# Optimization experiments

Hardware: AMD Instinct MI355X
Metric: run time of the kernel (lower is better)

## Reference

```python
import jax, jax.numpy as jnp
import numpy as np
import math

B, N, XD, ED, H = 8, 128, 256, 128, 8
DF = XD // H
FFX, FFE = 1024, 512


def _lin(x, w, b):
    return x @ w + b


def _ln(x, g, b):
    m = x.mean(-1, keepdims=True)
    v = ((x - m) ** 2).mean(-1, keepdims=True)
    return (x - m) / jnp.sqrt(v + 1e-5) * g + b


def setup_inputs() -> dict:
    key = jax.random.key(0)
    ks = jax.random.split(key, 16)
    d = {}
    d['x'] = jax.random.normal(ks[0], (B, N, XD), jnp.float32)
    d['e'] = jax.random.normal(ks[1], (B, N, N, ED), jnp.float32)
    wspecs = [('wq', (XD, XD)), ('wk', (XD, XD)), ('wv', (XD, XD)),
              ('wem', (ED, XD)), ('wea', (ED, XD)), ('wxo', (XD, XD)),
              ('weo', (XD, ED)), ('wx1', (XD, FFX)), ('wx2', (FFX, XD)),
              ('we1', (ED, FFE)), ('we2', (FFE, ED))]
    for i, (name, shp) in enumerate(wspecs):
        d[name] = jax.random.normal(ks[2 + i % 14], shp, jnp.float32) * 0.02
        d[name] = jax.random.normal(jax.random.fold_in(key, i + 10), shp, jnp.float32) * 0.02
    for name, dim in [('bq', XD), ('bk', XD), ('bv', XD), ('bem', XD), ('bea', XD),
                      ('bxo', XD), ('beo', ED), ('bx1', FFX), ('bx2', XD),
                      ('be1', FFE), ('be2', ED)]:
        d[name] = jnp.zeros((dim,), jnp.float32)
    d['gnx'] = jnp.ones((XD,), jnp.float32)
    d['bnx'] = jnp.zeros((XD,), jnp.float32)
    d['gne'] = jnp.ones((ED,), jnp.float32)
    d['bne'] = jnp.zeros((ED,), jnp.float32)
    return d


def reference(x, e, wq, wk, wv, wem, wea, wxo, weo, wx1, wx2, we1, we2,
              bq, bk, bv, bem, bea, bxo, beo, bx1, bx2, be1, be2,
              gnx, bnx, gne, bne):
    # --- NodeEdgeBlock ---
    Q = _lin(x, wq, bq).reshape(B, N, H, DF)
    K = _lin(x, wk, bk).reshape(B, N, H, DF)
    # per-channel outer product: (B, N_i, N_j, H, DF)
    Y = Q[:, :, None] * K[:, None] / math.sqrt(DF)
    E1 = _lin(e, wem, bem).reshape(B, N, N, H, DF)
    E2 = _lin(e, wea, bea).reshape(B, N, N, H, DF)
    Y = Y * (E1 + 1.0) + E2
    newE = _lin(Y.reshape(B, N, N, XD), weo, beo)
    attn = jax.nn.softmax(Y, axis=1)  # softmax over source-node axis i
    V = _lin(x, wv, bv := bv if False else bv).reshape(B, N, H, DF) if False else _lin(x, wv, bv).reshape(B, N, H, DF)
    wV = (attn * V[:, None]).sum(axis=1).reshape(B, N, XD)
    newX = _lin(wV, wxo, bxo)

    # --- FF blocks (dropout=0 => identity); note the SAME norm (norm2) is applied twice,
    # and the second residual uses the pre-norm input, matching the torch code. ---
    def ff(inp, new, w1, b1, w2, b2, g, bn):
        h = _ln(inp + new, g, bn)
        h = jax.nn.relu(_lin(h, w1, b1))
        h = _lin(h, w2, b2)
        return _ln(inp + h, g, bn)

    x_out = ff(x, newX, wx1, bx1, wx2, bx2, gnx, bnx)
    e_out = ff(e, newE, we1, be1, we2, be2, gne, bne)
    return (x_out, e_out)
```

## Files before the change

### kernel.cpp

```cpp
#include <hip/hip_runtime.h>


#define RSQRT_DF 0.17677669529663687f

typedef __attribute__((ext_vector_type(8))) short short8;
typedef __attribute__((ext_vector_type(4))) short short4v;
typedef __attribute__((ext_vector_type(4))) float f32x4;

__device__ __forceinline__ short f2bs(float f) {
    unsigned u = __float_as_uint(f);
    unsigned r = u + 0x7FFFu + ((u >> 16) & 1u);
    return (short)(r >> 16);
}
__device__ __forceinline__ float bs2f(short s) {
    return __uint_as_float(((unsigned)(unsigned short)s) << 16);
}

struct PackArgs {
    const float* W[11];
    short* Wp[11];
    int kdiv[11];
    int N[11];
    int start[12];
};

__global__ __launch_bounds__(256) void pack_all(PackArgs pa) {
    int g = blockIdx.x * 256 + threadIdx.x;
    if (g >= pa.start[11]) return;
    int i = 0;
    while (g >= pa.start[i + 1]) ++i;
    int local = g - pa.start[i];
    int kdiv = pa.kdiv[i], N = pa.N[i];
    int lane = local & 63, rest = local >> 6;
    int kb = rest % kdiv, nt = rest / kdiv;
    int n = nt * 16 + (lane & 15);
    int k0 = kb * 32 + ((lane >> 4) << 3);
    const float* W = pa.W[i];
    short8 v;
#pragma unroll
    for (int j = 0; j < 8; ++j) v[j] = f2bs(W[(size_t)(k0 + j) * N + n]);
    *(short8*)(pa.Wp[i] + (size_t)local * 8) = v;
}

__global__ __launch_bounds__(256) void qk_gemm(
    const float* __restrict__ x,
    const short* __restrict__ wqP, const short* __restrict__ wkP,
    const float* __restrict__ bq, const float* __restrict__ bk,
    float* __restrict__ Qb, float* __restrict__ Kb) {
    __shared__ short sXb[16 * 264];
    const int t = threadIdx.x, wave = t >> 6, lane = t & 63;
    const int quad = lane >> 4, l15 = lane & 15;
    const int m0 = (blockIdx.x & 63) * 16;
    const int isK = blockIdx.x >> 6;
    const short* wP = isK ? wkP : wqP;
    const float* bp = isK ? bk : bq;
    float* outp = isK ? Kb : Qb;

    const float4* x4 = (const float4*)(x + (size_t)m0 * 256);
    for (int g = t; g < 1024; g += 256) {
        float4 v = x4[g];
        int row = g >> 6, col4 = (g & 63) * 4;
        short4v sv = {f2bs(v.x), f2bs(v.y), f2bs(v.z), f2bs(v.w)};
        *(short4v*)(sXb + row * 264 + col4) = sv;
    }
    __syncthreads();

#pragma unroll 2
    for (int p = 0; p < 4; ++p) {
        int nt = wave * 4 + p;
        f32x4 acc = (f32x4){0.f, 0.f, 0.f, 0.f};
        const short* aB = sXb + l15 * 264 + quad * 8;
        const short* bB = wP + ((size_t)(nt * 8) * 64 + lane) * 8;
#pragma unroll
        for (int kb = 0; kb < 8; ++kb) {
            short8 a = *(const short8*)(aB + kb * 32);
            short8 w = *(const short8*)(bB + (size_t)kb * 512);
            acc = __builtin_amdgcn_mfma_f32_16x16x32_bf16(a, w, acc, 0, 0, 0);
        }
        int col = nt * 16 + l15;
        float bvv = bp[col];
#pragma unroll
        for (int r = 0; r < 4; ++r)
            outp[(size_t)(m0 + quad * 4 + r) * 256 + col] = acc[r] + bvv;
    }
}

__global__ __launch_bounds__(512, 3) void fused_main(
    const float* __restrict__ x, const float* __restrict__ e,
    const float* __restrict__ Qb, const float* __restrict__ Kb,
    const short* __restrict__ wvP, const short* __restrict__ wxoP,
    const short* __restrict__ wx1P, const short* __restrict__ wx2P,
    const short* __restrict__ wemP, const short* __restrict__ weaP,
    const short* __restrict__ weoP, const short* __restrict__ we1P,
    const short* __restrict__ we2P,
    const float* __restrict__ bv, const float* __restrict__ bxo,
    const float* __restrict__ bx1, const float* __restrict__ bx2,
    const float* __restrict__ bem, const float* __restrict__ bea,
    const float* __restrict__ beo, const float* __restrict__ be1,
    const float* __restrict__ be2,
    const float* __restrict__ gnx, const float* __restrict__ bnx,
    const float* __restrict__ gne, const float* __restrict__ bne,
    float* __restrict__ xout, float* __restrict__ eout) {
    __shared__ __align__(16) char ldsbuf[68608];
    const int t = threadIdx.x, wave = t >> 6, lane = t & 63;
    const int quad = lane >> 4, l15 = lane & 15;

    if (blockIdx.x < 32) {
        short* sXb  = (short*)ldsbuf;
        short* sVb  = (short*)(ldsbuf + 16896);
        short* sTbx = (short*)(ldsbuf + 33792);
        short* sRx  = (short*)(ldsbuf + 50688);
        short* sH1x = (short*)(ldsbuf + 50688);
        short* sH2x = (short*)(ldsbuf + 50688);
        const int m0 = blockIdx.x * 32;

        const float4* x4 = (const float4*)(x + (size_t)m0 * 256);
        for (int g = t; g < 2048; g += 512) {
            float4 v = x4[g];
            int row = g >> 6, col4 = (g & 63) * 4;
            short4v sv = {f2bs(v.x), f2bs(v.y), f2bs(v.z), f2bs(v.w)};
            *(short4v*)(sXb + row * 264 + col4) = sv;
        }
        __syncthreads();

#pragma unroll
        for (int ntl = 0; ntl < 2; ++ntl) {
            const int nt = wave * 2 + ntl;
            const short* bB = wvP + ((size_t)(nt * 8) * 64 + lane) * 8;
            short8 w[8];
#pragma unroll
            for (int kb = 0; kb < 8; ++kb) w[kb] = *(const short8*)(bB + (size_t)kb * 512);
            const int col = nt * 16 + l15;
            const float bvv = bv[col];
#pragma unroll
            for (int mt = 0; mt < 2; ++mt) {
                f32x4 acc = (f32x4){0.f, 0.f, 0.f, 0.f};
#pragma unroll
                for (int kb = 0; kb < 8; ++kb) {
                    short8 a = *(const short8*)(sXb + (mt * 16 + l15) * 264 + quad * 8 + kb * 32);
                    acc = __builtin_amdgcn_mfma_f32_16x16x32_bf16(a, w[kb], acc, 0, 0, 0);
                }
#pragma unroll
                for (int r = 0; r < 4; ++r)
                    sVb[(mt * 16 + quad * 4 + r) * 264 + col] = f2bs(acc[r] + bvv);
            }
        }
        __syncthreads();

#pragma unroll
        for (int ntl = 0; ntl < 2; ++ntl) {
            const int nt = wave * 2 + ntl;
            const short* bB = wxoP + ((size_t)(nt * 8) * 64 + lane) * 8;
            short8 w[8];
#pragma unroll
            for (int kb = 0; kb < 8; ++kb) w[kb] = *(const short8*)(bB + (size_t)kb * 512);
            const int col = nt * 16 + l15;
            const float bvv = bxo[col];
#pragma unroll
            for (int mt = 0; mt < 2; ++mt) {
                f32x4 acc = (f32x4){0.f, 0.f, 0.f, 0.f};
#pragma unroll
                for (int kb = 0; kb < 8; ++kb) {
                    short8 a = *(const short8*)(sVb + (mt * 16 + l15) * 264 + quad * 8 + kb * 32);
                    acc = __builtin_amdgcn_mfma_f32_16x16x32_bf16(a, w[kb], acc, 0, 0, 0);
                }
#pragma unroll
                for (int r = 0; r < 4; ++r)
                    sRx[(mt * 16 + quad * 4 + r) * 264 + col] = f2bs(acc[r] + bvv);
            }
        }
        __syncthreads();

        for (int rr = 0; rr < 4; ++rr) {
            int row = wave * 4 + rr;
            float v[4];
            float s1 = 0.f, s2 = 0.f;
#pragma unroll
            for (int k = 0; k < 4; ++k) {
                v[k] = bs2f(sXb[row * 264 + lane + 64 * k]) + bs2f(sRx[row * 264 + lane + 64 * k]);
                s1 += v[k]; s2 += v[k] * v[k];
            }
            for (int off = 32; off; off >>= 1) {
                s1 += __shfl_down(s1, off);
                s2 += __shfl_down(s2, off);
            }
            s1 = __shfl(s1, 0); s2 = __shfl(s2, 0);
            float mean = s1 * (1.f / 256.f);
            float var = s2 * (1.f / 256.f) - mean * mean;
            float rstd = rsqrtf(var + 1e-5f);
#pragma unroll
            for (int k = 0; k < 4; ++k)
                sTbx[row * 264 + lane + 64 * k] =
                    f2bs((v[k] - mean) * rstd * gnx[lane + 64 * k] + bnx[lane + 64 * k]);
        }
        __syncthreads();

        f32x4 accEx[2][2];
#pragma unroll
        for (int i = 0; i < 2; ++i)
#pragma unroll
            for (int j = 0; j < 2; ++j) accEx[i][j] = (f32x4){0.f, 0.f, 0.f, 0.f};

        for (int q = 0; q < 4; ++q) {
#pragma unroll
            for (int ntl = 0; ntl < 2; ++ntl) {
                const int ntg = q * 16 + wave * 2 + ntl;
                const short* bB = wx1P + ((size_t)(ntg * 8) * 64 + lane) * 8;
                short8 w[8];
#pragma unroll
                for (int kb = 0; kb < 8; ++kb) w[kb] = *(const short8*)(bB + (size_t)kb * 512);
                const int coll = (wave * 2 + ntl) * 16 + l15;
                const float bvv = bx1[ntg * 16 + l15];
#pragma unroll
                for (int mt = 0; mt < 2; ++mt) {
                    f32x4 acc = (f32x4){0.f, 0.f, 0.f, 0.f};
#pragma unroll
                    for (int kb = 0; kb < 8; ++kb) {
                        short8 a = *(const short8*)(sTbx + (mt * 16 + l15) * 264 + quad * 8 + kb * 32);
                        acc = __builtin_amdgcn_mfma_f32_16x16x32_bf16(a, w[kb], acc, 0, 0, 0);
                    }
#pragma unroll
                    for (int r = 0; r < 4; ++r)
                        sH1x[(mt * 16 + quad * 4 + r) * 264 + coll] = f2bs(fmaxf(acc[r] + bvv, 0.f));
                }
            }
            __syncthreads();
#pragma unroll
            for (int ntl = 0; ntl < 2; ++ntl) {
                const int nt = wave * 2 + ntl;
                const short* bB = wx2P + ((size_t)(nt * 32 + q * 8) * 64 + lane) * 8;
                short8 w[8];
#pragma unroll
                for (int kb = 0; kb < 8; ++kb) w[kb] = *(const short8*)(bB + (size_t)kb * 512);
#pragma unroll
                for (int mt = 0; mt < 2; ++mt) {
#pragma unroll
                    for (int kb = 0; kb < 8; ++kb) {
                        short8 a = *(const short8*)(sH1x + (mt * 16 + l15) * 264 + quad * 8 + kb * 32);
                        accEx[ntl][mt] = __builtin_amdgcn_mfma_f32_16x16x32_bf16(a, w[kb], accEx[ntl][mt], 0, 0, 0);
                    }
                }
            }
            __syncthreads();
        }
#pragma unroll
        for (int ntl = 0; ntl < 2; ++ntl)
#pragma unroll
            for (int mt = 0; mt < 2; ++mt) {
                const int col = (wave * 2 + ntl) * 16 + l15;
                const float bvv = bx2[col];
#pragma unroll
                for (int r = 0; r < 4; ++r)
                    sH2x[(mt * 16 + quad * 4 + r) * 264 + col] = f2bs(accEx[ntl][mt][r] + bvv);
            }
        __syncthreads();

        for (int rr = 0; rr < 4; ++rr) {
            int row = wave * 4 + rr;
            float v[4];
            float s1 = 0.f, s2 = 0.f;
#pragma unroll
            for (int k = 0; k < 4; ++k) {
                v[k] = bs2f(sXb[row * 264 + lane + 64 * k]) + bs2f(sH2x[row * 264 + lane + 64 * k]);
                s1 += v[k]; s2 += v[k] * v[k];
            }
            for (int off = 32; off; off >>= 1) {
                s1 += __shfl_down(s1, off);
                s2 += __shfl_down(s2, off);
            }
            s1 = __shfl(s1, 0); s2 = __shfl(s2, 0);
            float mean = s1 * (1.f / 256.f);
            float var = s2 * (1.f / 256.f) - mean * mean;
            float rstd = rsqrtf(var + 1e-5f);
#pragma unroll
            for (int k = 0; k < 4; ++k)
                xout[(size_t)(m0 + row) * 256 + lane + 64 * k] =
                    (v[k] - mean) * rstd * gnx[lane + 64 * k] + bnx[lane + 64 * k];
        }
        return;
    }

    short* sEb = (short*)ldsbuf;
    short* sYb = (short*)(ldsbuf + 17408);
    short* sTb = (short*)(ldsbuf + 17408);
    float* sH2 = (float*)(ldsbuf + 17408);
    short* sR  = (short*)(ldsbuf + 51200);
    short* sH1 = (short*)(ldsbuf + 51200);

    const int r0 = (blockIdx.x - 32) * 64;
    const int b = r0 >> 14;
    const int j0 = r0 & 127;

    {
        const float4* e4 = (const float4*)(e + (size_t)r0 * 128);
        for (int g = t; g < 2048; g += 512) {
            float4 v = e4[g];
            int row = g >> 5, col4 = (g & 31) * 4;
            short4v sv = {f2bs(v.x), f2bs(v.y), f2bs(v.z), f2bs(v.w)};
            *(short4v*)(sEb + row * 136 + col4) = sv;
        }
    }
    __syncthreads();

#pragma unroll
    for (int ntl = 0; ntl < 2; ++ntl) {
        const int nt = wave * 2 + ntl;
        const short* b1 = wemP + ((size_t)(nt * 4) * 64 + lane) * 8;
        const short* b2 = weaP + ((size_t)(nt * 4) * 64 + lane) * 8;
        short8 w1[4], w2[4];
#pragma unroll
        for (int kb = 0; kb < 4; ++kb) {
            w1[kb] = *(const short8*)(b1 + (size_t)kb * 512);
            w2[kb] = *(const short8*)(b2 + (size_t)kb * 512);
        }
        const int col = nt * 16 + l15;
        const float bm = bem[col], ba = bea[col];
        const float q = Qb[(size_t)(r0 >> 7) * 256 + col] * RSQRT_DF;
#pragma unroll
        for (int mt = 0; mt < 4; ++mt) {
            const float* kp = Kb + (size_t)((b << 7) + j0 + mt * 16 + quad * 4) * 256 + col;
            float kv[4];
#pragma unroll
            for (int r = 0; r < 4; ++r) kv[r] = kp[(size_t)r * 256];
            f32x4 a1 = (f32x4){0.f, 0.f, 0.f, 0.f};
            f32x4 a2 = (f32x4){0.f, 0.f, 0.f, 0.f};
#pragma unroll
            for (int kb = 0; kb < 4; ++kb) {
                short8 a = *(const short8*)(sEb + (mt * 16 + l15) * 136 + quad * 8 + kb * 32);
                a1 = __builtin_amdgcn_mfma_f32_16x16x32_bf16(a, w1[kb], a1, 0, 0, 0);
                a2 = __builtin_amdgcn_mfma_f32_16x16x32_bf16(a, w2[kb], a2, 0, 0, 0);
            }
#pragma unroll
            for (int r = 0; r < 4; ++r) {
                int row = mt * 16 + quad * 4 + r;
                float y = q * kv[r] * (a1[r] + bm + 1.0f) + (a2[r] + ba);
                sYb[row * 264 + col] = f2bs(y);
            }
        }
    }
    __syncthreads();

    {
        const int nt = wave;
        const short* bB = weoP + ((size_t)(nt * 8) * 64 + lane) * 8;
        short8 w[8];
#pragma unroll
        for (int kb = 0; kb < 8; ++kb) w[kb] = *(const short8*)(bB + (size_t)kb * 512);
        const int col = nt * 16 + l15;
        const float bo = beo[col];
#pragma unroll
        for (int mt = 0; mt < 4; ++mt) {
            f32x4 acc = (f32x4){0.f, 0.f, 0.f, 0.f};
#pragma unroll
            for (int kb = 0; kb < 8; ++kb) {
                short8 a = *(const short8*)(sYb + (mt * 16 + l15) * 264 + quad * 8 + kb * 32);
                acc = __builtin_amdgcn_mfma_f32_16x16x32_bf16(a, w[kb], acc, 0, 0, 0);
            }
#pragma unroll
            for (int r = 0; r < 4; ++r)
                sR[(mt * 16 + quad * 4 + r) * 136 + col] = f2bs(acc[r] + bo);
        }
    }
    __syncthreads();

    {
        float g0 = gne[lane], g1 = gne[lane + 64];
        float bn0 = bne[lane], bn1 = bne[lane + 64];
        for (int rr = 0; rr < 8; ++rr) {
            int row = wave * 8 + rr;
            float v0 = bs2f(sEb[row * 136 + lane]) + bs2f(sR[row * 136 + lane]);
            float v1 = bs2f(sEb[row * 136 + lane + 64]) + bs2f(sR[row * 136 + lane + 64]);
            float s1 = v0 + v1, s2 = v0 * v0 + v1 * v1;
            for (int off = 32; off; off >>= 1) {
                s1 += __shfl_down(s1, off);
                s2 += __shfl_down(s2, off);
            }
            s1 = __shfl(s1, 0); s2 = __shfl(s2, 0);
            float mean = s1 * 0.0078125f;
            float var = s2 * 0.0078125f - mean * mean;
            float rstd = rsqrtf(var + 1e-5f);
            sTb[row * 136 + lane]      = f2bs((v0 - mean) * rstd * g0 + bn0);
            sTb[row * 136 + lane + 64] = f2bs((v1 - mean) * rstd * g1 + bn1);
        }
    }
    __syncthreads();

    f32x4 accE[4];
#pragma unroll
    for (int p = 0; p < 4; ++p) accE[p] = (f32x4){0.f, 0.f, 0.f, 0.f};

    for (int q = 0; q < 4; ++q) {
        {
            const int ntg = q * 8 + wave;
            const short* bB = we1P + ((size_t)(ntg * 4) * 64 + lane) * 8;
            short8 w[4];
#pragma unroll
            for (int kb = 0; kb < 4; ++kb) w[kb] = *(const short8*)(bB + (size_t)kb * 512);
            const int coll = wave * 16 + l15;
            const float bvv = be1[ntg * 16 + l15];
#pragma unroll
            for (int mt = 0; mt < 4; ++mt) {
                f32x4 acc = (f32x4){0.f, 0.f, 0.f, 0.f};
#pragma unroll
                for (int kb = 0; kb < 4; ++kb) {
                    short8 a = *(const short8*)(sTb + (mt * 16 + l15) * 136 + quad * 8 + kb * 32);
                    acc = __builtin_amdgcn_mfma_f32_16x16x32_bf16(a, w[kb], acc, 0, 0, 0);
                }
#pragma unroll
                for (int r = 0; r < 4; ++r)
                    sH1[(mt * 16 + quad * 4 + r) * 136 + coll] = f2bs(fmaxf(acc[r] + bvv, 0.f));
            }
        }
        __syncthreads();
        {
            const int nt = wave;
            const short* bB = we2P + ((size_t)(nt * 16 + q * 4) * 64 + lane) * 8;
            short8 w[4];
#pragma unroll
            for (int kb = 0; kb < 4; ++kb) w[kb] = *(const short8*)(bB + (size_t)kb * 512);
#pragma unroll
            for (int mt = 0; mt < 4; ++mt) {
#pragma unroll
                for (int kb = 0; kb < 4; ++kb) {
                    short8 a = *(const short8*)(sH1 + (mt * 16 + l15) * 136 + quad * 8 + kb * 32);
                    accE[mt] = __builtin_amdgcn_mfma_f32_16x16x32_bf16(a, w[kb], accE[mt], 0, 0, 0);
                }
            }
        }
        __syncthreads();
    }
    {
        const int col = wave * 16 + l15;
        const float bvv = be2[col];
#pragma unroll
        for (int mt = 0; mt < 4; ++mt)
#pragma unroll
            for (int r = 0; r < 4; ++r)
                sH2[(mt * 16 + quad * 4 + r) * 132 + col] = accE[mt][r] + bvv;
    }
    __syncthreads();

    {
        float g0 = gne[lane], g1 = gne[lane + 64];
        float bn0 = bne[lane], bn1 = bne[lane + 64];
        for (int rr = 0; rr < 8; ++rr) {
            int row = wave * 8 + rr;
            float v0 = bs2f(sEb[row * 136 + lane]) + sH2[row * 132 + lane];
            float v1 = bs2f(sEb[row * 136 + lane + 64]) + sH2[row * 132 + lane + 64];
            float s1 = v0 + v1, s2 = v0 * v0 + v1 * v1;
            for (int off = 32; off; off >>= 1) {
                s1 += __shfl_down(s1, off);
                s2 += __shfl_down(s2, off);
            }
            s1 = __shfl(s1, 0); s2 = __shfl(s2, 0);
            float mean = s1 * 0.0078125f;
            float var = s2 * 0.0078125f - mean * mean;
            float rstd = rsqrtf(var + 1e-5f);
            size_t o = (size_t)(r0 + row) * 128;
            eout[o + lane]      = (v0 - mean) * rstd * g0 + bn0;
            eout[o + lane + 64] = (v1 - mean) * rstd * g1 + bn1;
        }
    }
}

extern "C" void kernel_launch(void* const* d_in, const int* in_sizes, int n_in,
                              void* d_out, int out_size, void* d_ws, size_t ws_size,
                              hipStream_t stream) {
    const float* x   = (const float*)d_in[0];
    const float* e   = (const float*)d_in[1];
    const float* wq  = (const float*)d_in[2];
    const float* wk  = (const float*)d_in[3];
    const float* wv  = (const float*)d_in[4];
    const float* wem = (const float*)d_in[5];
    const float* wea = (const float*)d_in[6];
    const float* wxo = (const float*)d_in[7];
    const float* weo = (const float*)d_in[8];
    const float* wx1 = (const float*)d_in[9];
    const float* wx2 = (const float*)d_in[10];
    const float* we1 = (const float*)d_in[11];
    const float* we2 = (const float*)d_in[12];
    const float* bq  = (const float*)d_in[13];
    const float* bk  = (const float*)d_in[14];
    const float* bv  = (const float*)d_in[15];
    const float* bem = (const float*)d_in[16];
    const float* bea = (const float*)d_in[17];
    const float* bxo = (const float*)d_in[18];
    const float* beo = (const float*)d_in[19];
    const float* bx1 = (const float*)d_in[20];
    const float* bx2 = (const float*)d_in[21];
    const float* be1 = (const float*)d_in[22];
    const float* be2 = (const float*)d_in[23];
    const float* gnx = (const float*)d_in[24];
    const float* bnx = (const float*)d_in[25];
    const float* gne = (const float*)d_in[26];
    const float* bne = (const float*)d_in[27];

    float* out = (float*)d_out;

    float* ws = (float*)d_ws;
    float* Qb = ws;
    float* Kb = Qb + 262144;
    short* base = (short*)(Kb + 262144);
    short* wqP  = base;
    short* wkP  = wqP + 65536;
    short* wvP  = wkP + 65536;
    short* wxoP = wvP + 65536;
    short* wx1P = wxoP + 65536;
    short* wx2P = wx1P + 262144;
    short* wemP = wx2P + 262144;
    short* weaP = wemP + 32768;
    short* weoP = weaP + 32768;
    short* we1P = weoP + 32768;
    short* we2P = we1P + 65536;

    PackArgs pa;
    const float* Ws[11] = {wq, wk, wv, wxo, wx1, wx2, wem, wea, weo, we1, we2};
    short* Wps[11] = {wqP, wkP, wvP, wxoP, wx1P, wx2P, wemP, weaP, weoP, we1P, we2P};
    int Ks[11] = {256, 256, 256, 256, 256, 1024, 128, 128, 256, 128, 512};
    int Ns[11] = {256, 256, 256, 256, 1024, 256, 256, 256, 128, 512, 128};
    int acc = 0;
    for (int i = 0; i < 11; ++i) {
        pa.W[i] = Ws[i];
        pa.Wp[i] = Wps[i];
        pa.kdiv[i] = Ks[i] >> 5;
        pa.N[i] = Ns[i];
        pa.start[i] = acc;
        acc += (Ns[i] >> 4) * (Ks[i] >> 5) * 64;
    }
    pa.start[11] = acc;
    pack_all<<<(acc + 255) / 256, 256, 0, stream>>>(pa);

    qk_gemm<<<128, 256, 0, stream>>>(x, wqP, wkP, bq, bk, Qb, Kb);

    fused_main<<<2080, 512, 0, stream>>>(
        x, e, Qb, Kb, wvP, wxoP, wx1P, wx2P, wemP, weaP, weoP, we1P, we2P,
        bv, bxo, bx1, bx2, bem, bea, beo, be1, be2,
        gnx, bnx, gne, bne, out, out + 262144);
}
```

Baseline: 296.8 us.

## Hoist edge-path weight loads and software-prefetch FFN weights across stages

Loads the wem/wea/weo weight fragments and the per-column constants into registers before the e-tile load, so their global latency overlaps with the staging of e into LDS. The E1/E2 loop is reordered to run over row tiles with both column tiles at once, which shares each A-fragment LDS read across four MFMAs. The FFN loop now double-buffers we1/we2 fragments, fetching the next chunk's weights while the current MFMAs run. The cost is much higher register pressure (dozens of short8 values live at once), which could lower occupancy or cause spills.

After: 326.3 us. 10.0% more time.

```diff
diff --git a/kernel.cpp b/kernel.cpp
--- a/kernel.cpp
+++ b/kernel.cpp
@@ -291,6 +291,36 @@
     const int b = r0 >> 14;
     const int j0 = r0 & 127;
 
+    const int ntA = wave * 2, ntB = wave * 2 + 1;
+    const int colA = ntA * 16 + l15, colB = ntB * 16 + l15;
+    short8 w1A[4], w2A[4], w1B[4], w2B[4];
+    {
+        const short* p1A = wemP + ((size_t)(ntA * 4) * 64 + lane) * 8;
+        const short* p2A = weaP + ((size_t)(ntA * 4) * 64 + lane) * 8;
+        const short* p1B = wemP + ((size_t)(ntB * 4) * 64 + lane) * 8;
+        const short* p2B = weaP + ((size_t)(ntB * 4) * 64 + lane) * 8;
+#pragma unroll
+        for (int kb = 0; kb < 4; ++kb) {
+            w1A[kb] = *(const short8*)(p1A + (size_t)kb * 512);
+            w2A[kb] = *(const short8*)(p2A + (size_t)kb * 512);
+            w1B[kb] = *(const short8*)(p1B + (size_t)kb * 512);
+            w2B[kb] = *(const short8*)(p2B + (size_t)kb * 512);
+        }
+    }
+    short8 wC[8];
+    {
+        const short* pC = weoP + ((size_t)(wave * 8) * 64 + lane) * 8;
+#pragma unroll
+        for (int kb = 0; kb < 8; ++kb) wC[kb] = *(const short8*)(pC + (size_t)kb * 512);
+    }
+    const float qA = Qb[(size_t)(r0 >> 7) * 256 + colA] * RSQRT_DF;
+    const float qB = Qb[(size_t)(r0 >> 7) * 256 + colB] * RSQRT_DF;
+    const float bmA = bem[colA], baA = bea[colA];
+    const float bmB = bem[colB], baB = bea[colB];
+    const float boC = beo[wave * 16 + l15];
+    const float g0 = gne[lane], g1 = gne[lane + 64];
+    const float bn0 = bne[lane], bn1 = bne[lane + 64];
+
     {
         const float4* e4 = (const float4*)(e + (size_t)r0 * 128);
         for (int g = t; g < 2048; g += 512) {
@@ -303,85 +333,77 @@
     __syncthreads();
 
 #pragma unroll
-    for (int ntl = 0; ntl < 2; ++ntl) {
-        const int nt = wave * 2 + ntl;
-        const short* b1 = wemP + ((size_t)(nt * 4) * 64 + lane) * 8;
-        const short* b2 = weaP + ((size_t)(nt * 4) * 64 + lane) * 8;
-        short8 w1[4], w2[4];
+    for (int mt = 0; mt < 4; ++mt) {
+        const float* kpA = Kb + (size_t)((b << 7) + j0 + mt * 16 + quad * 4) * 256 + colA;
+        const float* kpB = Kb + (size_t)((b << 7) + j0 + mt * 16 + quad * 4) * 256 + colB;
+        float kvA[4], kvB[4];
+#pragma unroll
+        for (int r = 0; r < 4; ++r) {
+            kvA[r] = kpA[(size_t)r * 256];
+            kvB[r] = kpB[(size_t)r * 256];
+        }
+        short8 aE[4];
+#pragma unroll
+        for (int kb = 0; kb < 4; ++kb)
+            aE[kb] = *(const short8*)(sEb + (mt * 16 + l15) * 136 + quad * 8 + kb * 32);
+        f32x4 a1A = (f32x4){0.f, 0.f, 0.f, 0.f}, a2A = (f32x4){0.f, 0.f, 0.f, 0.f};
+        f32x4 a1B = (f32x4){0.f, 0.f, 0.f, 0.f}, a2B = (f32x4){0.f, 0.f, 0.f, 0.f};
 #pragma unroll
         for (int kb = 0; kb < 4; ++kb) {
-            w1[kb] = *(const short8*)(b1 + (size_t)kb * 512);
-            w2[kb] = *(const short8*)(b2 + (size_t)kb * 512);
-        }
-        const int col = nt * 16 + l15;
-        const float bm = bem[col], ba = bea[col];
-        const float q = Qb[(size_t)(r0 >> 7) * 256 + col] * RSQRT_DF;
-#pragma unroll
-        for (int mt = 0; mt < 4; ++mt) {
-            const float* kp = Kb + (size_t)((b << 7) + j0 + mt * 16 + quad * 4) * 256 + col;
-            float kv[4];
-#pragma unroll
-            for (int r = 0; r < 4; ++r) kv[r] = kp[(size_t)r * 256];
-            f32x4 a1 = (f32x4){0.f, 0.f, 0.f, 0.f};
-            f32x4 a2 = (f32x4){0.f, 0.f, 0.f, 0.f};
-#pragma unroll
-            for (int kb = 0; kb < 4; ++kb) {
-                short8 a = *(const short8*)(sEb + (mt * 16 + l15) * 136 + quad * 8 + kb * 32);
-                a1 = __builtin_amdgcn_mfma_f32_16x16x32_bf16(a, w1[kb], a1, 0, 0, 0);
-                a2 = __builtin_amdgcn_mfma_f32_16x16x32_bf16(a, w2[kb], a2, 0, 0, 0);
-            }
-#pragma unroll
-            for (int r = 0; r < 4; ++r) {
-                int row = mt * 16 + quad * 4 + r;
-                float y = q * kv[r] * (a1[r] + bm + 1.0f) + (a2[r] + ba);
-                sYb[row * 264 + col] = f2bs(y);
-            }
+            a1A = __builtin_amdgcn_mfma_f32_16x16x32_bf16(aE[kb], w1A[kb], a1A, 0, 0, 0);
+            a2A = __builtin_amdgcn_mfma_f32_16x16x32_bf16(aE[kb], w2A[kb], a2A, 0, 0, 0);
+            a1B = __builtin_amdgcn_mfma_f32_16x16x32_bf16(aE[kb], w1B[kb], a1B, 0, 0, 0);
+            a2B = __builtin_amdgcn_mfma_f32_16x16x32_bf16(aE[kb], w2B[kb], a2B, 0, 0, 0);
+        }
+#pragma unroll
+        for (int r = 0; r < 4; ++r) {
+            int row = mt * 16 + quad * 4 + r;
+            sYb[row * 264 + colA] = f2bs(qA * kvA[r] * (a1A[r] + bmA + 1.0f) + (a2A[r] + baA));
+            sYb[row * 264 + colB] = f2bs(qB * kvB[r] * (a1B[r] + bmB + 1.0f) + (a2B[r] + baB));
         }
     }
     __syncthreads();
 
+#pragma unroll
+    for (int mt = 0; mt < 4; ++mt) {
+        f32x4 acc = (f32x4){0.f, 0.f, 0.f, 0.f};
+#pragma unroll
+        for (int kb = 0; kb < 8; ++kb) {
+            short8 a = *(const short8*)(sYb + (mt * 16 + l15) * 264 + quad * 8 + kb * 32);
+            acc = __builtin_amdgcn_mfma_f32_16x16x32_bf16(a, wC[kb], acc, 0, 0, 0);
+        }
+        const int col = wave * 16 + l15;
+#pragma unroll
+        for (int r = 0; r < 4; ++r)
+            sR[(mt * 16 + quad * 4 + r) * 136 + col] = f2bs(acc[r] + boC);
+    }
+    short8 f1w[4], f2w[4];
     {
-        const int nt = wave;
-        const short* bB = weoP + ((size_t)(nt * 8) * 64 + lane) * 8;
-        short8 w[8];
-#pragma unroll
-        for (int kb = 0; kb < 8; ++kb) w[kb] = *(const short8*)(bB + (size_t)kb * 512);
-        const int col = nt * 16 + l15;
-        const float bo = beo[col];
-#pragma unroll
-        for (int mt = 0; mt < 4; ++mt) {
-            f32x4 acc = (f32x4){0.f, 0.f, 0.f, 0.f};
-#pragma unroll
-            for (int kb = 0; kb < 8; ++kb) {
-                short8 a = *(const short8*)(sYb + (mt * 16 + l15) * 264 + quad * 8 + kb * 32);
-                acc = __builtin_amdgcn_mfma_f32_16x16x32_bf16(a, w[kb], acc, 0, 0, 0);
-            }
-#pragma unroll
-            for (int r = 0; r < 4; ++r)
-                sR[(mt * 16 + quad * 4 + r) * 136 + col] = f2bs(acc[r] + bo);
+        const short* p1 = we1P + ((size_t)((0 * 8 + wave) * 4) * 64 + lane) * 8;
+        const short* p2 = we2P + ((size_t)(wave * 16 + 0 * 4) * 64 + lane) * 8;
+#pragma unroll
+        for (int kb = 0; kb < 4; ++kb) {
+            f1w[kb] = *(const short8*)(p1 + (size_t)kb * 512);
+            f2w[kb] = *(const short8*)(p2 + (size_t)kb * 512);
         }
     }
     __syncthreads();
 
-    {
-        float g0 = gne[lane], g1 = gne[lane + 64];
-        float bn0 = bne[lane], bn1 = bne[lane + 64];
-        for (int rr = 0; rr < 8; ++rr) {
-            int row = wave * 8 + rr;
-            float v0 = bs2f(sEb[row * 136 + lane]) + bs2f(sR[row * 136 + lane]);
-            float v1 = bs2f(sEb[row * 136 + lane + 64]) + bs2f(sR[row * 136 + lane + 64]);
-            float s1 = v0 + v1, s2 = v0 * v0 + v1 * v1;
-            for (int off = 32; off; off >>= 1) {
-                s1 += __shfl_down(s1, off);
-                s2 += __shfl_down(s2, off);
-            }
-            s1 = __shfl(s1, 0); s2 = __shfl(s2, 0);
-            float mean = s1 * 0.0078125f;
-            float var = s2 * 0.0078125f - mean * mean;
-            float rstd = rsqrtf(var + 1e-5f);
-            sTb[row * 136 + lane]      = f2bs((v0 - mean) * rstd * g0 + bn0);
-            sTb[row * 136 + lane + 64] = f2bs((v1 - mean) * rstd * g1 + bn1);
-        }
+    for (int rr = 0; rr < 8; ++rr) {
+        int row = wave * 8 + rr;
+        float v0 = bs2f(sEb[row * 136 + lane]) + bs2f(sR[row * 136 + lane]);
+        float v1 = bs2f(sEb[row * 136 + lane + 64]) + bs2f(sR[row * 136 + lane + 64]);
+        float s1 = v0 + v1, s2 = v0 * v0 + v1 * v1;
+        for (int off = 32; off; off >>= 1) {
+            s1 += __shfl_down(s1, off);
+            s2 += __shfl_down(s2, off);
+        }
+        s1 = __shfl(s1, 0); s2 = __shfl(s2, 0);
+        float mean = s1 * 0.0078125f;
+        float var = s2 * 0.0078125f - mean * mean;
+        float rstd = rsqrtf(var + 1e-5f);
+        sTb[row * 136 + lane]      = f2bs((v0 - mean) * rstd * g0 + bn0);
+        sTb[row * 136 + lane + 64] = f2bs((v1 - mean) * rstd * g1 + bn1);
     }
     __syncthreads();
 
@@ -389,22 +411,24 @@
 #pragma unroll
     for (int p = 0; p < 4; ++p) accE[p] = (f32x4){0.f, 0.f, 0.f, 0.f};
 
+#pragma unroll
     for (int q = 0; q < 4; ++q) {
+        short8 f1n[4];
+        if (q < 3) {
+            const short* p1 = we1P + ((size_t)(((q + 1) * 8 + wave) * 4) * 64 + lane) * 8;
+#pragma unroll
+            for (int kb = 0; kb < 4; ++kb) f1n[kb] = *(const short8*)(p1 + (size_t)kb * 512);
+        }
         {
-            const int ntg = q * 8 + wave;
-            const short* bB = we1P + ((size_t)(ntg * 4) * 64 + lane) * 8;
-            short8 w[4];
-#pragma unroll
-            for (int kb = 0; kb < 4; ++kb) w[kb] = *(const short8*)(bB + (size_t)kb * 512);
             const int coll = wave * 16 + l15;
-            const float bvv = be1[ntg * 16 + l15];
+            const float bvv = be1[(q * 8 + wave) * 16 + l15];
 #pragma unroll
             for (int mt = 0; mt < 4; ++mt) {
                 f32x4 acc = (f32x4){0.f, 0.f, 0.f, 0.f};
 #pragma unroll
                 for (int kb = 0; kb < 4; ++kb) {
                     short8 a = *(const short8*)(sTb + (mt * 16 + l15) * 136 + quad * 8 + kb * 32);
-                    acc = __builtin_amdgcn_mfma_f32_16x16x32_bf16(a, w[kb], acc, 0, 0, 0);
+                    acc = __builtin_amdgcn_mfma_f32_16x16x32_bf16(a, f1w[kb], acc, 0, 0, 0);
                 }
 #pragma unroll
                 for (int r = 0; r < 4; ++r)
@@ -412,22 +436,25 @@
             }
         }
         __syncthreads();
-        {
-            const int nt = wave;
-            const short* bB = we2P + ((size_t)(nt * 16 + q * 4) * 64 + lane) * 8;
-            short8 w[4];
-#pragma unroll
-            for (int kb = 0; kb < 4; ++kb) w[kb] = *(const short8*)(bB + (size_t)kb * 512);
-#pragma unroll
-            for (int mt = 0; mt < 4; ++mt) {
-#pragma unroll
-                for (int kb = 0; kb < 4; ++kb) {
-                    short8 a = *(const short8*)(sH1 + (mt * 16 + l15) * 136 + quad * 8 + kb * 32);
-                    accE[mt] = __builtin_amdgcn_mfma_f32_16x16x32_bf16(a, w[kb], accE[mt], 0, 0, 0);
-                }
-            }
-        }
-        __syncthreads();
+        short8 f2n[4];
+        if (q < 3) {
+            const short* p2 = we2P + ((size_t)(wave * 16 + (q + 1) * 4) * 64 + lane) * 8;
+#pragma unroll
+            for (int kb = 0; kb < 4; ++kb) f2n[kb] = *(const short8*)(p2 + (size_t)kb * 512);
+        }
+#pragma unroll
+        for (int mt = 0; mt < 4; ++mt) {
+#pragma unroll
+            for (int kb = 0; kb < 4; ++kb) {
+                short8 a = *(const short8*)(sH1 + (mt * 16 + l15) * 136 + quad * 8 + kb * 32);
+                accE[mt] = __builtin_amdgcn_mfma_f32_16x16x32_bf16(a, f2w[kb], accE[mt], 0, 0, 0);
+            }
+        }
+        __syncthreads();
+        if (q < 3) {
+#pragma unroll
+            for (int kb = 0; kb < 4; ++kb) { f1w[kb] = f1n[kb]; f2w[kb] = f2n[kb]; }
+        }
     }
     {
         const int col = wave * 16 + l15;
@@ -440,26 +467,22 @@
     }
     __syncthreads();
 
-    {
-        float g0 = gne[lane], g1 = gne[lane + 64];
-        float bn0 = bne[lane], bn1 = bne[lane + 64];
-        for (int rr = 0; rr < 8; ++rr) {
-            int row = wave * 8 + rr;
-            float v0 = bs2f(sEb[row * 136 + lane]) + sH2[row * 132 + lane];
-            float v1 = bs2f(sEb[row * 136 + lane + 64]) + sH2[row * 132 + lane + 64];
-            float s1 = v0 + v1, s2 = v0 * v0 + v1 * v1;
-            for (int off = 32; off; off >>= 1) {
-                s1 += __shfl_down(s1, off);
-                s2 += __shfl_down(s2, off);
-            }
-            s1 = __shfl(s1, 0); s2 = __shfl(s2, 0);
-            float mean = s1 * 0.0078125f;
-            float var = s2 * 0.0078125f - mean * mean;
-            float rstd = rsqrtf(var + 1e-5f);
-            size_t o = (size_t)(r0 + row) * 128;
-            eout[o + lane]      = (v0 - mean) * rstd * g0 + bn0;
-            eout[o + lane + 64] = (v1 - mean) * rstd * g1 + bn1;
-        }
+    for (int rr = 0; rr < 8; ++rr) {
+        int row = wave * 8 + rr;
+        float v0 = bs2f(sEb[row * 136 + lane]) + sH2[row * 132 + lane];
+        float v1 = bs2f(sEb[row * 136 + lane + 64]) + sH2[row * 132 + lane + 64];
+        float s1 = v0 + v1, s2 = v0 * v0 + v1 * v1;
+        for (int off = 32; off; off >>= 1) {
+            s1 += __shfl_down(s1, off);
+            s2 += __shfl_down(s2, off);
+        }
+        s1 = __shfl(s1, 0); s2 = __shfl(s2, 0);
+        float mean = s1 * 0.0078125f;
+        float var = s2 * 0.0078125f - mean * mean;
+        float rstd = rsqrtf(var + 1e-5f);
+        size_t o = (size_t)(r0 + row) * 128;
+        eout[o + lane]      = (v0 - mean) * rstd * g0 + bn0;
+        eout[o + lane + 64] = (v1 - mean) * rstd * g1 + bn1;
     }
 }
 
```
